# Kernel optimization log

Hardware: AMD Instinct MI355X
Metric: run time of the kernel (lower is better)

## Reference

```python
import jax, jax.numpy as jnp
import numpy as np

PROJ = 8192     # projDim
THRESH = 1e-8   # numerical-stability epsilon for signed sqrt
L2_EPS = 1e-12  # eps of torch F.normalize


def setup_inputs() -> dict:
    key = jax.random.key(0)
    k1, k2, k3, k4, k5 = jax.random.split(key, 5)
    B, C, H, W = 16, 512, 14, 14
    x = jax.random.normal(k1, (B, C, H, W), dtype=jnp.float32)
    h1 = jax.random.randint(k2, (C,), 0, PROJ, dtype=jnp.int32)
    h2 = jax.random.randint(k3, (C,), 0, PROJ, dtype=jnp.int32)
    s1 = (2 * jax.random.randint(k4, (C,), 0, 2) - 1).astype(jnp.float32)
    s2 = (2 * jax.random.randint(k5, (C,), 0, 2) - 1).astype(jnp.float32)
    return {"x": x, "s1": s1, "s2": s2, "h1": h1, "h2": h2}


def reference(x, s1, s2, h1, h2):
    # x: [B, C, H, W]; h*: [C] hash buckets in [0, PROJ); s*: [C] signs (+-1)
    B, C, H, W = x.shape
    x_flat = jnp.transpose(x, (0, 2, 3, 1)).reshape(-1, C)  # [N, C], N = B*H*W

    def count_sketch(s, h):
        # Equivalent to x_flat @ M with M[c, h[c]] = s[c]: scatter-add of
        # sign-weighted channels into PROJ bins.  -> [N, PROJ]
        return jax.ops.segment_sum((x_flat * s).T, h, num_segments=PROJ).T

    fft1 = jnp.fft.fft(count_sketch(s1, h1), axis=-1)
    fft2 = jnp.fft.fft(count_sketch(s2, h2), axis=-1)
    conv = jnp.fft.ifft(fft1 * fft2, axis=-1).real       # [N, PROJ]
    y = conv.reshape(B, H, W, PROJ).sum(axis=(1, 2))      # sum pool -> [B, PROJ]
    y = jnp.sign(y) * jnp.sqrt(jnp.abs(y) + THRESH)       # signed sqrt
    norm = jnp.linalg.norm(y, axis=1, keepdims=True)
    return y / jnp.maximum(norm, L2_EPS)                  # l2 normalize (dim=1)
```

## Files before the change

kernel.cpp:

```cpp
#include <hip/hip_runtime.h>
#include <math.h>

#define PROJ 8192
#define NB   16
#define NC   512
#define HW   196
#define KP   224
#define LST  40
#define XELE ((size_t)NB * NC * KP)

typedef __attribute__((ext_vector_type(8))) short bf16x8;
typedef __attribute__((ext_vector_type(4))) short short4v;
typedef __attribute__((ext_vector_type(4))) float f32x4;

__device__ __forceinline__ unsigned bf16_rne(float f) {
    unsigned u = __builtin_bit_cast(unsigned, f);
    return (u + 0x7fffu + ((u >> 16) & 1u)) >> 16;
}

__global__ __launch_bounds__(256)
void cbp_prep(const float* __restrict__ x,
              short* __restrict__ xh, short* __restrict__ xl) {
    const int id  = blockIdx.x * 256 + threadIdx.x;
    const int q   = id % 56;
    const int row = id / 56;
    float4 v = {0.f, 0.f, 0.f, 0.f};
    if (q < 49) v = *(const float4*)&x[(size_t)row * HW + 4 * q];
    const float f[4] = {v.x, v.y, v.z, v.w};
    short4v h, l;
#pragma unroll
    for (int c = 0; c < 4; ++c) {
        const unsigned hb = bf16_rne(f[c]);
        h[c] = (short)hb;
        l[c] = (short)bf16_rne(f[c] - __builtin_bit_cast(float, hb << 16));
    }
    *(short4v*)&xh[(size_t)row * KP + 4 * q] = h;
    *(short4v*)&xl[(size_t)row * KP + 4 * q] = l;
}

__global__ __launch_bounds__(512, 2)
void cbp_gram(const short* __restrict__ xh, const short* __restrict__ xl,
              const float* __restrict__ s1, const float* __restrict__ s2,
              const int*   __restrict__ h1, const int*   __restrict__ h2,
              float* __restrict__ partials) {
    __shared__ float sk[PROJ];
    __shared__ short Ah[128 * LST];
    __shared__ short Al[128 * LST];
    __shared__ short Bh[128 * LST];
    __shared__ short Bl[128 * LST];
    __shared__ int   lh1[128], lh2[128];
    __shared__ float ls1[128], ls2[128];

    const int tid = threadIdx.x;
    const int blk = blockIdx.x;
    const int xcd = blk & 7;
    const int hi  = blk >> 7;
    const int b   = 2 * xcd + hi;
    const int tile = (blk >> 3) & 15;
    const int I = tile >> 2, J = tile & 3;
    const int c1base = I * 128, c2base = J * 128;

    for (int i = tid; i < PROJ; i += 512) sk[i] = 0.f;
    if (tid < 128) {
        lh1[tid] = h1[c1base + tid];  ls1[tid] = s1[c1base + tid];
    } else if (tid < 256) {
        const int t = tid - 128;
        lh2[t] = h2[c2base + t];  ls2[t] = s2[c2base + t];
    }

    const int wave = tid >> 6, lane = tid & 63;
    const int quad = lane >> 4, l15 = lane & 15;
    const int wr = (wave >> 1) * 32;
    const int wc = (wave & 1) * 64;

    const int sr = tid >> 2;
    const int sl = tid & 3;

    const size_t baseA = ((size_t)b * NC + c1base + sr) * KP + sl * 8;
    const size_t baseB = ((size_t)b * NC + c2base + sr) * KP + sl * 8;

    bf16x8 pAh, pAl, pBh, pBl;
    pAh = *(const bf16x8*)&xh[baseA];
    pAl = *(const bf16x8*)&xl[baseA];
    pBh = *(const bf16x8*)&xh[baseB];
    pBl = *(const bf16x8*)&xl[baseB];

    f32x4 acc[2][4];
#pragma unroll
    for (int i = 0; i < 2; ++i)
#pragma unroll
        for (int j = 0; j < 4; ++j) acc[i][j] = (f32x4){0.f, 0.f, 0.f, 0.f};

    for (int kc = 0; kc < 7; ++kc) {
        __syncthreads();
        *(bf16x8*)&Ah[sr * LST + sl * 8] = pAh;
        *(bf16x8*)&Al[sr * LST + sl * 8] = pAl;
        *(bf16x8*)&Bh[sr * LST + sl * 8] = pBh;
        *(bf16x8*)&Bl[sr * LST + sl * 8] = pBl;
        if (kc < 6) {
            const size_t off = (size_t)(kc + 1) * 32;
            pAh = *(const bf16x8*)&xh[baseA + off];
            pAl = *(const bf16x8*)&xl[baseA + off];
            pBh = *(const bf16x8*)&xh[baseB + off];
            pBl = *(const bf16x8*)&xl[baseB + off];
        }
        __syncthreads();

        bf16x8 ahf[2], alf[2], bhf[4], blf[4];
#pragma unroll
        for (int i = 0; i < 2; ++i) {
            const int ra = wr + i * 16 + l15;
            ahf[i] = *(const bf16x8*)&Ah[ra * LST + quad * 8];
            alf[i] = *(const bf16x8*)&Al[ra * LST + quad * 8];
        }
#pragma unroll
        for (int j = 0; j < 4; ++j) {
            const int rb = wc + j * 16 + l15;
            bhf[j] = *(const bf16x8*)&Bh[rb * LST + quad * 8];
            blf[j] = *(const bf16x8*)&Bl[rb * LST + quad * 8];
        }
#pragma unroll
        for (int i = 0; i < 2; ++i)
#pragma unroll
            for (int j = 0; j < 4; ++j) {
                acc[i][j] = __builtin_amdgcn_mfma_f32_16x16x32_bf16(ahf[i], bhf[j], acc[i][j], 0, 0, 0);
                acc[i][j] = __builtin_amdgcn_mfma_f32_16x16x32_bf16(ahf[i], blf[j], acc[i][j], 0, 0, 0);
                acc[i][j] = __builtin_amdgcn_mfma_f32_16x16x32_bf16(alf[i], bhf[j], acc[i][j], 0, 0, 0);
            }
    }

#pragma unroll
    for (int i = 0; i < 2; ++i) {
        const int r0 = wr + i * 16 + quad * 4;
#pragma unroll
        for (int j = 0; j < 4; ++j) {
            const int c = wc + j * 16 + l15;
            const int h2v = lh2[c];
            const float s2v = ls2[c];
#pragma unroll
            for (int rg = 0; rg < 4; ++rg) {
                const int r = r0 + rg;
                const int bin = (lh1[r] + h2v) & (PROJ - 1);
                atomicAdd(&sk[bin], ls1[r] * s2v * acc[i][j][rg]);
            }
        }
    }
    __syncthreads();

    float4* dst = (float4*)(partials + (size_t)blk * PROJ);
    const float4* src = (const float4*)sk;
    for (int i = tid; i < PROJ / 4; i += 512) dst[i] = src[i];
}

__global__ __launch_bounds__(256)
void cbp_reduce(const float* __restrict__ partials, float* __restrict__ y,
                float* __restrict__ ssqp) {
    const int blk = blockIdx.x;
    const int xcd = blk & 7;
    const int k   = blk >> 3;
    const int hi  = k >> 5;
    const int seg = k & 31;
    const int b   = 2 * xcd + hi;
    const int tid = threadIdx.x;
    const int bin = seg * 256 + tid;

    float s = 0.f;
#pragma unroll
    for (int u = 0; u < 16; ++u) {
        const int u2 = (u + seg) & 15;
        const int pb = xcd | (u2 << 3) | (hi << 7);
        s += partials[(size_t)pb * PROJ + bin];
    }

    const float m = sqrtf(fabsf(s) + 1e-8f);
    const float o = (s > 0.f) ? m : (s < 0.f ? -m : 0.f);
    y[b * PROJ + bin] = o;

    __shared__ float red[256];
    red[tid] = o * o;
    __syncthreads();
#pragma unroll
    for (int st = 128; st >= 1; st >>= 1) {
        if (tid < st) red[tid] += red[tid + st];
        __syncthreads();
    }
    if (tid == 0) ssqp[blk] = red[0];
}

__global__ __launch_bounds__(256)
void cbp_normalize(float* __restrict__ y, const float* __restrict__ ssqp) {
    const int b   = blockIdx.x >> 1;
    const int off = (blockIdx.x & 1) * 4096;
    const int tid = threadIdx.x;
    float ssq = 0.f;
#pragma unroll
    for (int seg = 0; seg < 32; ++seg)
        ssq += ssqp[(((b & 1) * 32 + seg) << 3) | (b >> 1)];
    const float inv = 1.0f / fmaxf(sqrtf(ssq), 1e-12f);

    float4* row = (float4*)&y[(size_t)b * PROJ + off];
#pragma unroll
    for (int j = 0; j < 4; ++j) {
        float4 v = row[j * 256 + tid];
        v.x *= inv; v.y *= inv; v.z *= inv; v.w *= inv;
        row[j * 256 + tid] = v;
    }
}

extern "C" void kernel_launch(void* const* d_in, const int* in_sizes, int n_in,
                              void* d_out, int out_size, void* d_ws, size_t ws_size,
                              hipStream_t stream) {
    const float* x  = (const float*)d_in[0];
    const float* s1 = (const float*)d_in[1];
    const float* s2 = (const float*)d_in[2];
    const int*   h1 = (const int*)d_in[3];
    const int*   h2 = (const int*)d_in[4];
    float* y = (float*)d_out;

    short* xh = (short*)d_ws;
    short* xl = xh + XELE;
    float* partials = (float*)(xl + XELE);
    float* ssqp = partials + (size_t)256 * PROJ;

    hipLaunchKernelGGL(cbp_prep, dim3(1792), dim3(256), 0, stream, x, xh, xl);
    hipLaunchKernelGGL(cbp_gram, dim3(256), dim3(512), 0, stream,
                       xh, xl, s1, s2, h1, h2, partials);
    hipLaunchKernelGGL(cbp_reduce, dim3(512), dim3(256), 0, stream,
                       partials, y, ssqp);
    hipLaunchKernelGGL(cbp_normalize, dim3(32), dim3(256), 0, stream, y, ssqp);
}
```

Measured before the change: 105.4 us.

## Split gram tiles to 128x64 across 512 smaller blocks with XCD-aware prep mapping

The Gram/sketch kernel now runs 512 blocks of 256 threads, each computing a 128x64 channel tile instead of 256 blocks of 512 threads on 128x128 tiles. The intent is to fill more compute units and improve latency hiding. The reduce kernel is changed to sum 32 partial sketches per batch. The prep kernel's block-to-row mapping is changed to group rows by XCD, and the hash and sign values are hoisted into registers before the atomic scatter. The trade-off is twice as many per-block 8192-bin LDS sketches to zero, write out and reduce, which doubles the partials memory traffic.

```diff
diff --git a/kernel.cpp b/kernel.cpp
--- a/kernel.cpp
+++ b/kernel.cpp
@@ -21,9 +21,12 @@
 __global__ __launch_bounds__(256)
 void cbp_prep(const float* __restrict__ x,
               short* __restrict__ xh, short* __restrict__ xl) {
-    const int id  = blockIdx.x * 256 + threadIdx.x;
-    const int q   = id % 56;
-    const int row = id / 56;
+    const int e    = blockIdx.x & 7;
+    const int t    = blockIdx.x >> 3;
+    const int task = t * 256 + threadIdx.x;
+    const int q    = task % 56;
+    const int rp   = task / 56;
+    const int row  = e * 1024 + rp;
     float4 v = {0.f, 0.f, 0.f, 0.f};
     if (q < 49) v = *(const float4*)&x[(size_t)row * HW + 4 * q];
     const float f[4] = {v.x, v.y, v.z, v.w};
@@ -38,7 +41,7 @@
     *(short4v*)&xl[(size_t)row * KP + 4 * q] = l;
 }
 
-__global__ __launch_bounds__(512, 2)
+__global__ __launch_bounds__(256)
 void cbp_gram(const short* __restrict__ xh, const short* __restrict__ xl,
               const float* __restrict__ s1, const float* __restrict__ s2,
               const int*   __restrict__ h1, const int*   __restrict__ h2,
@@ -46,44 +49,44 @@
     __shared__ float sk[PROJ];
     __shared__ short Ah[128 * LST];
     __shared__ short Al[128 * LST];
-    __shared__ short Bh[128 * LST];
-    __shared__ short Bl[128 * LST];
-    __shared__ int   lh1[128], lh2[128];
-    __shared__ float ls1[128], ls2[128];
+    __shared__ short Bh[64 * LST];
+    __shared__ short Bl[64 * LST];
+    __shared__ int   lh1[128], lh2[64];
+    __shared__ float ls1[128], ls2[64];
 
     const int tid = threadIdx.x;
     const int blk = blockIdx.x;
     const int xcd = blk & 7;
-    const int hi  = blk >> 7;
+    const int tj  = (blk >> 3) & 31;
+    const int hi  = blk >> 8;
     const int b   = 2 * xcd + hi;
-    const int tile = (blk >> 3) & 15;
-    const int I = tile >> 2, J = tile & 3;
-    const int c1base = I * 128, c2base = J * 128;
-
-    for (int i = tid; i < PROJ; i += 512) sk[i] = 0.f;
+    const int I   = tj >> 3, J = tj & 7;
+    const int c1base = I * 128, c2base = J * 64;
+
+    for (int i = tid; i < PROJ; i += 256) sk[i] = 0.f;
     if (tid < 128) {
         lh1[tid] = h1[c1base + tid];  ls1[tid] = s1[c1base + tid];
-    } else if (tid < 256) {
+    } else {
         const int t = tid - 128;
-        lh2[t] = h2[c2base + t];  ls2[t] = s2[c2base + t];
+        if (t < 64) { lh2[t] = h2[c2base + t];  ls2[t] = s2[c2base + t]; }
     }
 
     const int wave = tid >> 6, lane = tid & 63;
     const int quad = lane >> 4, l15 = lane & 15;
-    const int wr = (wave >> 1) * 32;
-    const int wc = (wave & 1) * 64;
-
-    const int sr = tid >> 2;
-    const int sl = tid & 3;
-
-    const size_t baseA = ((size_t)b * NC + c1base + sr) * KP + sl * 8;
-    const size_t baseB = ((size_t)b * NC + c2base + sr) * KP + sl * 8;
-
-    bf16x8 pAh, pAl, pBh, pBl;
-    pAh = *(const bf16x8*)&xh[baseA];
-    pAl = *(const bf16x8*)&xl[baseA];
-    pBh = *(const bf16x8*)&xh[baseB];
-    pBl = *(const bf16x8*)&xl[baseB];
+    const int wr = wave * 32;
+
+    const int arow0 = tid >> 2,  aslot0 = tid & 3;
+    const int arow1 = (256 + tid) >> 2, aslot1 = tid & 3;
+    const int brow  = tid >> 2,  bslot = tid & 3;
+
+    const size_t bA0 = ((size_t)b * NC + c1base + arow0) * KP + aslot0 * 8;
+    const size_t bA1 = ((size_t)b * NC + c1base + arow1) * KP + aslot1 * 8;
+    const size_t bB  = ((size_t)b * NC + c2base + brow ) * KP + bslot  * 8;
+
+    bf16x8 pa0h, pa0l, pa1h, pa1l, pbh, pbl;
+    pa0h = *(const bf16x8*)&xh[bA0];  pa0l = *(const bf16x8*)&xl[bA0];
+    pa1h = *(const bf16x8*)&xh[bA1];  pa1l = *(const bf16x8*)&xl[bA1];
+    pbh  = *(const bf16x8*)&xh[bB];   pbl  = *(const bf16x8*)&xl[bB];
 
     f32x4 acc[2][4];
 #pragma unroll
@@ -93,16 +96,17 @@
 
     for (int kc = 0; kc < 7; ++kc) {
         __syncthreads();
-        *(bf16x8*)&Ah[sr * LST + sl * 8] = pAh;
-        *(bf16x8*)&Al[sr * LST + sl * 8] = pAl;
-        *(bf16x8*)&Bh[sr * LST + sl * 8] = pBh;
-        *(bf16x8*)&Bl[sr * LST + sl * 8] = pBl;
+        *(bf16x8*)&Ah[arow0 * LST + aslot0 * 8] = pa0h;
+        *(bf16x8*)&Al[arow0 * LST + aslot0 * 8] = pa0l;
+        *(bf16x8*)&Ah[arow1 * LST + aslot1 * 8] = pa1h;
+        *(bf16x8*)&Al[arow1 * LST + aslot1 * 8] = pa1l;
+        *(bf16x8*)&Bh[brow * LST + bslot * 8]   = pbh;
+        *(bf16x8*)&Bl[brow * LST + bslot * 8]   = pbl;
         if (kc < 6) {
             const size_t off = (size_t)(kc + 1) * 32;
-            pAh = *(const bf16x8*)&xh[baseA + off];
-            pAl = *(const bf16x8*)&xl[baseA + off];
-            pBh = *(const bf16x8*)&xh[baseB + off];
-            pBl = *(const bf16x8*)&xl[baseB + off];
+            pa0h = *(const bf16x8*)&xh[bA0 + off];  pa0l = *(const bf16x8*)&xl[bA0 + off];
+            pa1h = *(const bf16x8*)&xh[bA1 + off];  pa1l = *(const bf16x8*)&xl[bA1 + off];
+            pbh  = *(const bf16x8*)&xh[bB  + off];  pbl  = *(const bf16x8*)&xl[bB  + off];
         }
         __syncthreads();
 
@@ -115,7 +119,7 @@
         }
 #pragma unroll
         for (int j = 0; j < 4; ++j) {
-            const int rb = wc + j * 16 + l15;
+            const int rb = j * 16 + l15;
             bhf[j] = *(const bf16x8*)&Bh[rb * LST + quad * 8];
             blf[j] = *(const bf16x8*)&Bl[rb * LST + quad * 8];
         }
@@ -129,27 +133,34 @@
             }
     }
 
-#pragma unroll
-    for (int i = 0; i < 2; ++i) {
-        const int r0 = wr + i * 16 + quad * 4;
-#pragma unroll
-        for (int j = 0; j < 4; ++j) {
-            const int c = wc + j * 16 + l15;
-            const int h2v = lh2[c];
-            const float s2v = ls2[c];
+    int   ha[8], hb[4];
+    float sa[8], sb[4];
+#pragma unroll
+    for (int i = 0; i < 2; ++i)
+#pragma unroll
+        for (int rg = 0; rg < 4; ++rg) {
+            const int r = wr + i * 16 + quad * 4 + rg;
+            ha[i * 4 + rg] = lh1[r];  sa[i * 4 + rg] = ls1[r];
+        }
+#pragma unroll
+    for (int j = 0; j < 4; ++j) {
+        const int c = j * 16 + l15;
+        hb[j] = lh2[c];  sb[j] = ls2[c];
+    }
+#pragma unroll
+    for (int i = 0; i < 2; ++i)
+#pragma unroll
+        for (int j = 0; j < 4; ++j)
 #pragma unroll
             for (int rg = 0; rg < 4; ++rg) {
-                const int r = r0 + rg;
-                const int bin = (lh1[r] + h2v) & (PROJ - 1);
-                atomicAdd(&sk[bin], ls1[r] * s2v * acc[i][j][rg]);
+                const int bin = (ha[i * 4 + rg] + hb[j]) & (PROJ - 1);
+                atomicAdd(&sk[bin], sa[i * 4 + rg] * sb[j] * acc[i][j][rg]);
             }
-        }
-    }
     __syncthreads();
 
     float4* dst = (float4*)(partials + (size_t)blk * PROJ);
     const float4* src = (const float4*)sk;
-    for (int i = tid; i < PROJ / 4; i += 512) dst[i] = src[i];
+    for (int i = tid; i < PROJ / 4; i += 256) dst[i] = src[i];
 }
 
 __global__ __launch_bounds__(256)
@@ -166,9 +177,9 @@
 
     float s = 0.f;
 #pragma unroll
-    for (int u = 0; u < 16; ++u) {
-        const int u2 = (u + seg) & 15;
-        const int pb = xcd | (u2 << 3) | (hi << 7);
+    for (int u = 0; u < 32; ++u) {
+        const int u2 = (u + seg) & 31;
+        const int pb = xcd | (u2 << 3) | (hi << 8);
         s += partials[(size_t)pb * PROJ + bin];
     }
 
@@ -195,7 +206,7 @@
     float ssq = 0.f;
 #pragma unroll
     for (int seg = 0; seg < 32; ++seg)
-        ssq += ssqp[(((b & 1) * 32 + seg) << 3) | (b >> 1)];
+        ssq += ssqp[(b >> 1) | (((b & 1) * 32 + seg) << 3)];
     const float inv = 1.0f / fmaxf(sqrtf(ssq), 1e-12f);
 
     float4* row = (float4*)&y[(size_t)b * PROJ + off];
@@ -220,10 +231,10 @@
     short* xh = (short*)d_ws;
     short* xl = xh + XELE;
     float* partials = (float*)(xl + XELE);
-    float* ssqp = partials + (size_t)256 * PROJ;
+    float* ssqp = partials + (size_t)512 * PROJ;
 
     hipLaunchKernelGGL(cbp_prep, dim3(1792), dim3(256), 0, stream, x, xh, xl);
-    hipLaunchKernelGGL(cbp_gram, dim3(256), dim3(512), 0, stream,
+    hipLaunchKernelGGL(cbp_gram, dim3(512), dim3(256), 0, stream,
                        xh, xl, s1, s2, h1, h2, partials);
     hipLaunchKernelGGL(cbp_reduce, dim3(512), dim3(256), 0, stream,
                        partials, y, ssqp);
```

Measured after the change: 108.0 us. 1.03x slower.
